# Kernel tuning notes

Hardware: AMD Instinct MI355X
Metric: run time of the kernel (lower is better)

The kernel has to match this reference:

```python
import jax, jax.numpy as jnp
import numpy as np

WS = 7      # window_size
NH = 8      # num_heads
ND = 5      # n_degree -> Np = 6


def setup_inputs() -> dict:
    key = jax.random.key(0)
    ks = jax.random.split(key, 9)
    B, Q, C, H, W = 2, 100, 256, 64, 64
    Np = ND + 1
    ws2 = WS * WS
    return {
        "x": jax.random.normal(ks[0], (B, C, H, W), dtype=jnp.float32),
        "polys": jax.random.uniform(ks[1], (B, Q, 2, Np), dtype=jnp.float32),
        "w_qkv": jax.random.normal(ks[2], (3 * C, C), dtype=jnp.float32) * 0.02,
        "b_qkv": jnp.zeros((3 * C,), dtype=jnp.float32),
        "w_proj": jax.random.normal(ks[3], (C, C), dtype=jnp.float32) * 0.02,
        "b_proj": jnp.zeros((C,), dtype=jnp.float32),
        "conv_w": jax.random.normal(ks[4], (1, ws2, 1, 1), dtype=jnp.float32) * 0.1,
        "conv_b": jnp.zeros((1,), dtype=jnp.float32),
        "pos_bias": jax.random.normal(ks[5], (ws2, 1), dtype=jnp.float32),
    }


def reference(x, polys, w_qkv, b_qkv, w_proj, b_proj, conv_w, conv_b, pos_bias):
    B, C, H, W = x.shape
    _, Q, _, Np = polys.shape  # polys: [B,Q,2,n_degree+1]
    ws = WS
    ws2 = ws * ws
    nh = NH
    hd = C // nh
    scale = hd ** -0.5

    # --- polynomial -> sample points (get_points) ---
    alpha = jnp.linspace(0.0, 1.0, Np)
    alphas = jnp.stack([alpha ** i for i in range(Np - 1, -1, -1)], axis=1)  # [Np, Np]
    points = jnp.swapaxes(polys @ alphas.T, -1, -2)  # [B,Q,Np,2]
    points = 2.0 * points - 1.0
    points = points[:, :, None, :, :]  # [B,Q,1,Np,2]

    # --- deformable window grid (faithful to torch, incl. -ws//2 floor-div) ---
    lo = (-ws) // 2   # -4 for ws=7
    hi = ws // 2      #  3
    delta_h = 2.0 * jnp.linspace(lo, hi, ws) / H
    delta_w = 2.0 * jnp.linspace(lo, hi, ws) / W
    mesh_x, mesh_y = jnp.meshgrid(delta_w, delta_h, indexing='xy')  # [ws,ws]
    mesh_x = mesh_x.reshape(-1, 1)  # [ws2,1]
    mesh_y = mesh_y.reshape(-1, 1)
    grid_y = points[..., 0] + mesh_y  # [B,Q,ws2,Np]
    grid_x = points[..., 1] + mesh_x
    grid = jnp.stack((grid_y, grid_x), axis=-1)        # [B,Q,ws2,Np,2]
    grid = grid.reshape(B, Q * Np * ws2, 2)            # same flat order as torch .view

    # --- grid_sample: bilinear, zeros padding, align_corners=True ---
    # grid[...,0] -> x coordinate (width), grid[...,1] -> y (height)
    def sample_one(img, g):  # img [C,H,W], g [P,2] -> [C,P]
        fx = (g[:, 0] + 1.0) * 0.5 * (W - 1)
        fy = (g[:, 1] + 1.0) * 0.5 * (H - 1)
        x0 = jnp.floor(fx)
        y0 = jnp.floor(fy)
        wx1 = fx - x0
        wy1 = fy - y0

        def gather(yy, xx):
            valid = (xx >= 0) & (xx <= W - 1) & (yy >= 0) & (yy <= H - 1)
            xi = jnp.clip(xx, 0, W - 1).astype(jnp.int32)
            yi = jnp.clip(yy, 0, H - 1).astype(jnp.int32)
            return img[:, yi, xi] * valid.astype(img.dtype)  # [C,P]

        v00 = gather(y0, x0)
        v01 = gather(y0, x0 + 1)
        v10 = gather(y0 + 1, x0)
        v11 = gather(y0 + 1, x0 + 1)
        return (v00 * (1 - wy1) * (1 - wx1) + v01 * (1 - wy1) * wx1 +
                v10 * wy1 * (1 - wx1) + v11 * wy1 * wx1)

    sampled = jax.vmap(sample_one)(x, grid)            # [B, C, Q*Np*ws2]
    sampled = sampled.reshape(B, C, Q * Np, ws2)
    sampled = jnp.transpose(sampled, (0, 2, 1, 3))     # [B, Q*Np, C, ws2]
    sp = sampled.reshape(B, Q, Np, C, ws2)
    sp = jnp.transpose(sp, (0, 1, 2, 4, 3)).reshape(B, Q * Np, ws2, C)

    # --- windowed multi-head self-attention over each sampled patch ---
    qkv = sp @ w_qkv.T + b_qkv                          # [B,QN,ws2,3C]
    qkv = qkv.reshape(B, Q * Np, ws2, 3, nh, hd)
    qkv = jnp.transpose(qkv, (3, 0, 4, 1, 2, 5))        # [3,B,nh,QN,ws2,hd]
    q, k, v = qkv[0], qkv[1], qkv[2]
    attn = jnp.einsum('bhnpd,bhnqd->bhnpq', q, k) * scale
    attn = attn + pos_bias.reshape(1, 1, 1, ws2, 1)     # bias per query row (as in torch)
    attn = jax.nn.softmax(attn, axis=-1)
    o = jnp.einsum('bhnpq,bhnqd->bhnpd', attn, v)       # [B,nh,QN,ws2,hd]
    o = jnp.swapaxes(o, 2, 3)                           # [B,nh,ws2,QN,hd]
    o = o.reshape(B, Q * Np, ws2, C)                    # faithful torch .reshape
    o = jnp.swapaxes(o, 1, 2)                           # [B,ws2,QN,C]

    # --- conv1x1 over the ws2 channel axis, then output projection ---
    y = jnp.einsum('bwnc,w->bnc', o, conv_w.reshape(ws2)) + conv_b.reshape(1, 1, 1)
    y = y @ w_proj.T + b_proj                           # [B,QN,C]
    return y.reshape(B, Q, Np, C)
```

## Files before the change

kernel.cpp:

```cpp
#include <hip/hip_runtime.h>
#include <hip/hip_bf16.h>

#define B_    2
#define QN    100
#define NP    6
#define WS2   49
#define CC    256
#define NHH   8
#define HDD   32
#define NWIN  600
#define O_PER_B 7526400

#define XT_BYTES   (8388608 + 1024)
#define ZABS       2097152
#define WB_BYTES   393216
#define WPT_BYTES  262144
#define QKV_SHORTS_PER_WIN (WS2 * 768)
#define QKV_BYTES  (1200 * WS2 * 768 * 2)

#define SPB_LD 264
#define CW_LD  72

typedef __attribute__((ext_vector_type(8))) short bf16x8;
typedef __attribute__((ext_vector_type(4))) float f32x4;

__device__ __forceinline__ unsigned short f2bf(float f) {
  union { float f; unsigned int i; } v; v.f = f;
  unsigned int x = v.i;
  x += 0x7fffu + ((x >> 16) & 1u);
  return (unsigned short)(x >> 16);
}
__device__ __forceinline__ float bf2f(unsigned short u) {
  union { unsigned int i; float f; } v; v.i = ((unsigned int)u) << 16; return v.f;
}

__global__ void k0_prep(const float* __restrict__ x, float* __restrict__ xT,
                        const float* __restrict__ w_qkv, unsigned short* __restrict__ wbp,
                        const float* __restrict__ w_proj, float* __restrict__ wpT) {
  __shared__ float tile[32][33];
  const int gb = blockIdx.x;
  if (gb < 2048) {
    int b   = gb >> 10;
    int rem = gb & 1023;
    int hw0 = (rem & 127) * 32;
    int c0  = (rem >> 7) * 32;
    int tx = threadIdx.x & 31, ty = threadIdx.x >> 5;
    const float* src = x + (size_t)b * CC * 4096;
    float* dst = xT + (size_t)b * 4096 * CC;
    #pragma unroll
    for (int i = ty; i < 32; i += 8)
      tile[i][tx] = src[(size_t)(c0 + i) * 4096 + hw0 + tx];
    __syncthreads();
    #pragma unroll
    for (int i = ty; i < 32; i += 8)
      dst[(size_t)(hw0 + i) * CC + c0 + tx] = tile[tx][i];
  } else if (gb < 2144) {
    int g = (gb - 2048) * 256 + threadIdx.x;
    int lane = g & 63;
    int ks = (g >> 6) & 7;
    int nt = g >> 9;
    int n  = nt * 16 + (lane & 15);
    int k0 = ks * 32 + (lane >> 4) * 8;
    const float* src = w_qkv + (size_t)n * CC + k0;
    float4 lo = *(const float4*)(src);
    float4 hi = *(const float4*)(src + 4);
    unsigned short o[8] = { f2bf(lo.x), f2bf(lo.y), f2bf(lo.z), f2bf(lo.w),
                            f2bf(hi.x), f2bf(hi.y), f2bf(hi.z), f2bf(hi.w) };
    *(uint4*)(wbp + (size_t)g * 8) = *(uint4*)o;
  } else if (gb == 2144) {
    xT[ZABS + threadIdx.x] = 0.0f;
  } else {
    int t = gb - 2145;
    int r0 = (t >> 3) * 32;
    int c0 = (t & 7) * 32;
    int tx = threadIdx.x & 31, ty = threadIdx.x >> 5;
    #pragma unroll
    for (int i = ty; i < 32; i += 8)
      tile[i][tx] = w_proj[(size_t)(r0 + i) * CC + c0 + tx];
    __syncthreads();
    #pragma unroll
    for (int i = ty; i < 32; i += 8)
      wpT[(size_t)(c0 + i) * CC + r0 + tx] = tile[tx][i];
  }
}

__launch_bounds__(256, 3)
__global__ void k1_sample_qkv(const float* __restrict__ xT,
                              const float* __restrict__ polys,
                              const unsigned short* __restrict__ wbp,
                              const float* __restrict__ b_qkv,
                              unsigned short* __restrict__ qkv_ws) {
  __shared__ __align__(16) unsigned short spb[64 * SPB_LD];
  __shared__ __align__(16) unsigned short Cwbuf[4][16 * CW_LD];
  __shared__ __align__(16) int   co_off[WS2][4];
  __shared__ __align__(16) float co_w[WS2][4];
  const int tid = threadIdx.x;
  const int m = blockIdx.x;
  const int b = blockIdx.y;

  if (tid < WS2) {
    int n = m * WS2 + tid;
    int q = n / (WS2 * NP);
    int p = (n / NP) % WS2;
    int a = n % NP;
    const float* pc = polys + (size_t)(b * QN + q) * 12;
    float al = (float)a * 0.2f;
    float py = pc[0];
    float px = pc[6];
    #pragma unroll
    for (int i = 1; i < 6; i++) { py = py * al + pc[i]; px = px * al + pc[6 + i]; }
    py = 2.0f * py - 1.0f;
    px = 2.0f * px - 1.0f;
    float gy = py + (2.0f * (-4.0f + (float)(p / 7) * (7.0f / 6.0f))) * (1.0f / 64.0f);
    float gx = px + (2.0f * (-4.0f + (float)(p % 7) * (7.0f / 6.0f))) * (1.0f / 64.0f);
    float fx = (gy + 1.0f) * 0.5f * 63.0f;
    float fy = (gx + 1.0f) * 0.5f * 63.0f;
    float x0 = floorf(fx), y0 = floorf(fy);
    float wx = fx - x0, wy = fy - y0;
    float x1 = x0 + 1.0f, y1 = y0 + 1.0f;
    int xi0 = (int)fminf(fmaxf(x0, 0.0f), 63.0f);
    int yi0 = (int)fminf(fmaxf(y0, 0.0f), 63.0f);
    int xi1 = (int)fminf(fmaxf(x1, 0.0f), 63.0f);
    int yi1 = (int)fminf(fmaxf(y1, 0.0f), 63.0f);
    bool vx0 = (x0 >= 0.0f) && (x0 <= 63.0f);
    bool vx1 = (x1 >= 0.0f) && (x1 <= 63.0f);
    bool vy0 = (y0 >= 0.0f) && (y0 <= 63.0f);
    bool vy1 = (y1 >= 0.0f) && (y1 <= 63.0f);
    const int bb = b * 4096;
    co_off[tid][0] = (vx0 && vy0) ? (bb + yi0 * 64 + xi0) * CC : ZABS;
    co_off[tid][1] = (vx1 && vy0) ? (bb + yi0 * 64 + xi1) * CC : ZABS;
    co_off[tid][2] = (vx0 && vy1) ? (bb + yi1 * 64 + xi0) * CC : ZABS;
    co_off[tid][3] = (vx1 && vy1) ? (bb + yi1 * 64 + xi1) * CC : ZABS;
    co_w[tid][0] = (1.0f - wy) * (1.0f - wx);
    co_w[tid][1] = (1.0f - wy) * wx;
    co_w[tid][2] = wy * (1.0f - wx);
    co_w[tid][3] = wy * wx;
  }
  {
    unsigned int* z = (unsigned int*)(spb + WS2 * SPB_LD);
    for (int i = tid; i < 15 * SPB_LD / 2; i += 256) z[i] = 0u;
  }
  __syncthreads();

  for (int bi = 0; bi < 12; bi++) {
    const int rbase = bi * 4;
    float vv[4][4];
    #pragma unroll
    for (int k = 0; k < 4; k++) {
      int r = rbase + k;
      int4 off = *(const int4*)&co_off[r][0];
      vv[k][0] = xT[off.x + tid];
      vv[k][1] = xT[off.y + tid];
      vv[k][2] = xT[off.z + tid];
      vv[k][3] = xT[off.w + tid];
    }
    #pragma unroll
    for (int k = 0; k < 4; k++) {
      int r = rbase + k;
      float4 w = *(const float4*)&co_w[r][0];
      float s = vv[k][0] * w.x + vv[k][1] * w.y + vv[k][2] * w.z + vv[k][3] * w.w;
      spb[r * SPB_LD + tid] = f2bf(s);
    }
  }
  {
    int4 off = *(const int4*)&co_off[48][0];
    float4 w = *(const float4*)&co_w[48][0];
    float s = xT[off.x + tid] * w.x + xT[off.y + tid] * w.y
            + xT[off.z + tid] * w.z + xT[off.w + tid] * w.w;
    spb[48 * SPB_LD + tid] = f2bf(s);
  }
  __syncthreads();

  const int lane = tid & 63;
  const int wv = tid >> 6;
  const int lm = lane & 15;
  const int lg = lane >> 4;
  unsigned short* qd = qkv_ws + (size_t)(b * NWIN + m) * QKV_SHORTS_PER_WIN;
  unsigned short* Cw = &Cwbuf[wv][0];

  for (int jc = 0; jc < 3; jc++) {
    const int nt0 = wv * 12 + jc * 4;
    const int ncol0 = nt0 * 16 + lm;
    f32x4 acc[4][4];
    #pragma unroll
    for (int j4 = 0; j4 < 4; j4++) {
      float bias = b_qkv[ncol0 + j4 * 16];
      #pragma unroll
      for (int mt = 0; mt < 4; mt++) acc[mt][j4] = (f32x4){bias, bias, bias, bias};
    }
    bf16x8 bnx[4];
    #pragma unroll
    for (int j4 = 0; j4 < 4; j4++)
      bnx[j4] = *(const bf16x8*)(wbp + (size_t)(((nt0 + j4) * 8 + 0) * 64 + lane) * 8);
    #pragma unroll
    for (int ks = 0; ks < 8; ks++) {
      bf16x8 bc[4];
      #pragma unroll
      for (int j4 = 0; j4 < 4; j4++) bc[j4] = bnx[j4];
      if (ks < 7) {
        #pragma unroll
        for (int j4 = 0; j4 < 4; j4++)
          bnx[j4] = *(const bf16x8*)(wbp + (size_t)(((nt0 + j4) * 8 + ks + 1) * 64 + lane) * 8);
      }
      bf16x8 af[4];
      #pragma unroll
      for (int mt = 0; mt < 4; mt++)
        af[mt] = *(const bf16x8*)(spb + (mt * 16 + lm) * SPB_LD + ks * 32 + lg * 8);
      #pragma unroll
      for (int j4 = 0; j4 < 4; j4++)
        #pragma unroll
        for (int mt = 0; mt < 4; mt++)
          acc[mt][j4] = __builtin_amdgcn_mfma_f32_16x16x32_bf16(af[mt], bc[j4], acc[mt][j4], 0, 0, 0);
    }
    const int cbase = nt0 * 16;
    #pragma unroll
    for (int mt = 0; mt < 4; mt++) {
      #pragma unroll
      for (int reg = 0; reg < 4; reg++) {
        int rr = lg * 4 + reg;
        #pragma unroll
        for (int j4 = 0; j4 < 4; j4++)
          Cw[rr * CW_LD + j4 * 16 + lm] = f2bf(acc[mt][j4][reg]);
      }
      int r0 = mt * 16;
      #pragma unroll
      for (int half = 0; half < 2; half++) {
        int idx = half * 64 + lane;
        int r16 = idx >> 3;
        int seg = idx & 7;
        int r = r0 + r16;
        if (r < WS2)
          *(uint4*)(qd + (size_t)r * 768 + cbase + seg * 8) =
              *(const uint4*)(Cw + r16 * CW_LD + seg * 8);
      }
    }
  }
}

#define P_LD 72
#define V_LD 72
#define OW_LD 36
#define P_WAVE (WS2 * P_LD)
#define V_OFF  (4 * P_WAVE)
#define V_WAVE (32 * V_LD)

__device__ __forceinline__ void attn_head(
    const bf16x8 qf[4], const bf16x8 kf[4],
    unsigned short* P, unsigned short* Vt, float* Ow, unsigned short* ob16,
    int lane, int lm, int lg) {
  const float scale = 0.17677669529663687f;
  f32x4 s[4][4];
  #pragma unroll
  for (int mt = 0; mt < 4; mt++)
    #pragma unroll
    for (int nt = 0; nt < 4; nt++) {
      s[mt][nt] = (f32x4){0.f, 0.f, 0.f, 0.f};
      s[mt][nt] = __builtin_amdgcn_mfma_f32_16x16x32_bf16(qf[mt], kf[nt], s[mt][nt], 0, 0, 0);
    }
  #pragma unroll
  for (int mt = 0; mt < 4; mt++)
    #pragma unroll
    for (int nt = 0; nt < 4; nt++) {
      bool badcol = (nt == 3) && (lm > 0);
      #pragma unroll
      for (int reg = 0; reg < 4; reg++)
        s[mt][nt][reg] = badcol ? -1e30f : s[mt][nt][reg] * scale;
    }
  #pragma unroll
  for (int mt = 0; mt < 4; mt++) {
    #pragma unroll
    for (int reg = 0; reg < 4; reg++) {
      float mx = fmaxf(fmaxf(s[mt][0][reg], s[mt][1][reg]),
                       fmaxf(s[mt][2][reg], s[mt][3][reg]));
      #pragma unroll
      for (int off = 1; off < 16; off <<= 1) mx = fmaxf(mx, __shfl_xor(mx, off));
      float sum = 0.0f;
      #pragma unroll
      for (int nt = 0; nt < 4; nt++) {
        float e = __expf(s[mt][nt][reg] - mx);
        s[mt][nt][reg] = e;
        sum += e;
      }
      #pragma unroll
      for (int off = 1; off < 16; off <<= 1) sum += __shfl_xor(sum, off);
      float inv = 1.0f / sum;
      #pragma unroll
      for (int nt = 0; nt < 4; nt++) s[mt][nt][reg] *= inv;
    }
  }
  #pragma unroll
  for (int mt = 0; mt < 4; mt++)
    #pragma unroll
    for (int nt = 0; nt < 4; nt++)
      #pragma unroll
      for (int reg = 0; reg < 4; reg++) {
        int p = mt * 16 + lg * 4 + reg;
        if (p < WS2) P[p * P_LD + nt * 16 + lm] = f2bf(s[mt][nt][reg]);
      }
  f32x4 o[4][2];
  #pragma unroll
  for (int mt = 0; mt < 4; mt++)
    #pragma unroll
    for (int nt2 = 0; nt2 < 2; nt2++) o[mt][nt2] = (f32x4){0.f, 0.f, 0.f, 0.f};
  #pragma unroll
  for (int ks = 0; ks < 2; ks++) {
    bf16x8 vf[2];
    #pragma unroll
    for (int nt2 = 0; nt2 < 2; nt2++)
      vf[nt2] = *(const bf16x8*)(Vt + (nt2 * 16 + lm) * V_LD + ks * 32 + lg * 8);
    #pragma unroll
    for (int mt = 0; mt < 4; mt++) {
      bf16x8 af = *(const bf16x8*)(P + (mt * 16 + lm) * P_LD + ks * 32 + lg * 8);
      #pragma unroll
      for (int nt2 = 0; nt2 < 2; nt2++)
        o[mt][nt2] = __builtin_amdgcn_mfma_f32_16x16x32_bf16(af, vf[nt2], o[mt][nt2], 0, 0, 0);
    }
  }
  #pragma unroll
  for (int mt = 0; mt < 4; mt++)
    #pragma unroll
    for (int reg = 0; reg < 4; reg++) {
      int p = mt * 16 + lg * 4 + reg;
      if (p < WS2) {
        #pragma unroll
        for (int nt2 = 0; nt2 < 2; nt2++)
          Ow[p * OW_LD + nt2 * 16 + lm] = o[mt][nt2][reg];
      }
    }
  for (int idx = lane; idx < WS2 * 4; idx += 64) {
    int p = idx >> 2, seg = idx & 3;
    const float* src = Ow + p * OW_LD + seg * 8;
    unsigned short o8[8];
    #pragma unroll
    for (int k = 0; k < 8; k++) o8[k] = f2bf(src[k]);
    *(uint4*)(ob16 + (size_t)idx * 8) = *(uint4*)o8;
  }
}

__launch_bounds__(256, 3)
__global__ void k2_attn(const unsigned short* __restrict__ qkv_ws,
                        unsigned short* __restrict__ o16) {
  __shared__ __align__(16) unsigned short lds[V_OFF + 4 * V_WAVE];
  const int tid = threadIdx.x;
  const int lane = tid & 63;
  const int wv = tid >> 6;
  const int lm = lane & 15;
  const int lg = lane >> 4;
  const int m = blockIdx.x;
  const int b = blockIdx.y;
  const unsigned short* wsrc = qkv_ws + (size_t)(b * NWIN + m) * QKV_SHORTS_PER_WIN;
  unsigned short* P  = lds + wv * P_WAVE;
  unsigned short* Vt = lds + V_OFF + wv * V_WAVE;
  float* Ow = (float*)P;

  {
    unsigned int* vz = (unsigned int*)Vt;
    #pragma unroll
    for (int i = 0; i < 18; i++) vz[i * 64 + lane] = 0u;
  }

  const int h0 = 2 * wv, h1 = 2 * wv + 1;
  const int vr = lane >> 2;
  const int vd0 = (lane & 3) * 8;
  uint4 vbuf[4];
  #pragma unroll
  for (int i = 0; i < 4; i++) {
    int r = vr + i * 16;
    int rc = (r > 48) ? 48 : r;
    vbuf[i] = *(const uint4*)(wsrc + (size_t)rc * 768 + 512 + h0 * HDD + vd0);
  }
  bf16x8 qf[2][4], kf[2][4];
  #pragma unroll
  for (int t = 0; t < 4; t++) {
    int r = t * 16 + lm; if (r > 48) r = 48;
    qf[0][t] = *(const bf16x8*)(wsrc + (size_t)r * 768 + h0 * HDD + lg * 8);
    kf[0][t] = *(const bf16x8*)(wsrc + (size_t)r * 768 + 256 + h0 * HDD + lg * 8);
    qf[1][t] = *(const bf16x8*)(wsrc + (size_t)r * 768 + h1 * HDD + lg * 8);
    kf[1][t] = *(const bf16x8*)(wsrc + (size_t)r * 768 + 256 + h1 * HDD + lg * 8);
  }
  #pragma unroll
  for (int i = 0; i < 4; i++) {
    int r = vr + i * 16;
    if (r < WS2) {
      unsigned int uu[4] = { vbuf[i].x, vbuf[i].y, vbuf[i].z, vbuf[i].w };
      #pragma unroll
      for (int k = 0; k < 4; k++) {
        Vt[(vd0 + 2 * k) * V_LD + r]     = (unsigned short)(uu[k] & 0xffffu);
        Vt[(vd0 + 2 * k + 1) * V_LD + r] = (unsigned short)(uu[k] >> 16);
      }
    }
  }

  unsigned short* obase = o16 + ((size_t)(b * NWIN + m) * 392) * 32;
  unsigned short* ob0 = obase + (size_t)h0 * WS2 * HDD;
  unsigned short* ob1 = obase + (size_t)h1 * WS2 * HDD;

  uint4 vbuf2[4];
  #pragma unroll
  for (int i = 0; i < 4; i++) {
    int r = vr + i * 16;
    int rc = (r > 48) ? 48 : r;
    vbuf2[i] = *(const uint4*)(wsrc + (size_t)rc * 768 + 512 + h1 * HDD + vd0);
  }

  attn_head(qf[0], kf[0], P, Vt, Ow, ob0, lane, lm, lg);

  #pragma unroll
  for (int i = 0; i < 4; i++) {
    int r = vr + i * 16;
    if (r < WS2) {
      unsigned int uu[4] = { vbuf2[i].x, vbuf2[i].y, vbuf2[i].z, vbuf2[i].w };
      #pragma unroll
      for (int k = 0; k < 4; k++) {
        Vt[(vd0 + 2 * k) * V_LD + r]     = (unsigned short)(uu[k] & 0xffffu);
        Vt[(vd0 + 2 * k + 1) * V_LD + r] = (unsigned short)(uu[k] >> 16);
      }
    }
  }

  attn_head(qf[1], kf[1], P, Vt, Ow, ob1, lane, lm, lg);
}

__global__ void k3_conv_proj(const unsigned short* __restrict__ o16,
                             const float* __restrict__ conv_w,
                             const float* __restrict__ conv_b,
                             const float* __restrict__ wpT,
                             const float* __restrict__ b_proj,
                             float* __restrict__ out) {
  __shared__ float yv[CC];
  __shared__ float cw[WS2];
  __shared__ int atab[392];
  const int tid = threadIdx.x;
  const int np = blockIdx.x;
  const int b = blockIdx.y;
  if (tid < WS2) cw[tid] = conv_w[tid];
  for (int i = tid; i < 392; i += 256) {
    int Q = np * 392 + i;
    int m = Q % 600;
    int hp = Q / 600;
    atab[i] = ((b * NWIN + m) * 392 + hp) * 32;
  }
  __syncthreads();
  const int cg = tid >> 5, dd = tid & 31;
  float acc = conv_b[0];
  for (int p = 0; p < WS2; p++)
    acc += cw[p] * bf2f(o16[(size_t)atab[p * 8 + cg] + dd]);
  yv[tid] = acc;
  __syncthreads();
  const float* wp = wpT + tid;
  float a0 = 0.0f, a1 = 0.0f, a2 = 0.0f, a3 = 0.0f;
  #pragma unroll 8
  for (int c = 0; c < CC; c += 4) {
    float4 y4 = *(const float4*)&yv[c];
    a0 += y4.x * wp[(c + 0) * CC];
    a1 += y4.y * wp[(c + 1) * CC];
    a2 += y4.z * wp[(c + 2) * CC];
    a3 += y4.w * wp[(c + 3) * CC];
  }
  out[((size_t)(b * NWIN + np)) * CC + tid] = b_proj[tid] + ((a0 + a1) + (a2 + a3));
}

extern "C" void kernel_launch(void* const* d_in, const int* in_sizes, int n_in,
                              void* d_out, int out_size, void* d_ws, size_t ws_size,
                              hipStream_t stream) {
  const float* x        = (const float*)d_in[0];
  const float* polys    = (const float*)d_in[1];
  const float* w_qkv    = (const float*)d_in[2];
  const float* b_qkv    = (const float*)d_in[3];
  const float* w_proj   = (const float*)d_in[4];
  const float* b_proj   = (const float*)d_in[5];
  const float* conv_w   = (const float*)d_in[6];
  const float* conv_b   = (const float*)d_in[7];
  float* out = (float*)d_out;

  char* ws = (char*)d_ws;
  float* xT = (float*)ws;
  unsigned short* wbp = (unsigned short*)(ws + XT_BYTES);
  float* wpT = (float*)(ws + XT_BYTES + WB_BYTES);
  unsigned short* qkv_ws = (unsigned short*)(ws + XT_BYTES + WB_BYTES + WPT_BYTES);
  unsigned short* o16 = (unsigned short*)(ws + XT_BYTES + WB_BYTES + WPT_BYTES + QKV_BYTES);

  hipLaunchKernelGGL(k0_prep, dim3(2209), dim3(256), 0, stream, x, xT, w_qkv, wbp, w_proj, wpT);
  hipLaunchKernelGGL(k1_sample_qkv, dim3(NWIN, B_), dim3(256), 0, stream,
                     xT, polys, wbp, b_qkv, qkv_ws);
  hipLaunchKernelGGL(k2_attn, dim3(NWIN, B_), dim3(256), 0, stream,
                     qkv_ws, o16);
  hipLaunchKernelGGL(k3_conv_proj, dim3(NWIN, B_), dim3(256), 0, stream,
                     o16, conv_w, conv_b, wpT, b_proj, out);
}
```

Before: 170.9 us.

## Fuse sampling/QKV projection with windowed attention, keeping QKV in LDS

Merges the sample+QKV kernel and the attention kernel into one, so each wave computes the Q/K/V columns for its own two heads and keeps them in shared memory, with V stored transposed directly from the accumulators. This removes the global round-trip of the bf16 QKV buffer (about 58 MB written and read back) and one kernel launch. The sampling loop also batches 8 rows of gathers instead of 4 to raise memory-level parallelism. In exchange LDS use per block grows and launch bounds drop to one block per SIMD group hint, which may lower occupancy.

```diff
diff --git a/kernel.cpp b/kernel.cpp
--- a/kernel.cpp
+++ b/kernel.cpp
@@ -1,5 +1,4 @@
 #include <hip/hip_runtime.h>
-#include <hip/hip_bf16.h>
 
 #define B_    2
 #define QN    100
@@ -9,17 +8,20 @@
 #define NHH   8
 #define HDD   32
 #define NWIN  600
-#define O_PER_B 7526400
 
 #define XT_BYTES   (8388608 + 1024)
 #define ZABS       2097152
 #define WB_BYTES   393216
 #define WPT_BYTES  262144
-#define QKV_SHORTS_PER_WIN (WS2 * 768)
-#define QKV_BYTES  (1200 * WS2 * 768 * 2)
 
 #define SPB_LD 264
-#define CW_LD  72
+
+#define QW_LD  136
+#define VT_LD  72
+#define P_LD   72
+#define OW_LD  36
+#define QW_SHORTS   (WS2 * QW_LD)
+#define WREG_SHORTS (QW_SHORTS + 64 * VT_LD)
 
 typedef __attribute__((ext_vector_type(8))) short bf16x8;
 typedef __attribute__((ext_vector_type(4))) float f32x4;
@@ -84,19 +86,118 @@
   }
 }
 
-__launch_bounds__(256, 3)
-__global__ void k1_sample_qkv(const float* __restrict__ xT,
-                              const float* __restrict__ polys,
-                              const unsigned short* __restrict__ wbp,
-                              const float* __restrict__ b_qkv,
-                              unsigned short* __restrict__ qkv_ws) {
+__device__ __forceinline__ void attn_head(
+    const bf16x8 qf[4], const bf16x8 kf[4],
+    unsigned short* P, const unsigned short* Vt, float* Ow, unsigned short* ob16,
+    int lane, int lm, int lg) {
+  const float scale = 0.17677669529663687f;
+  f32x4 s[4][4];
+  #pragma unroll
+  for (int mt = 0; mt < 4; mt++)
+    #pragma unroll
+    for (int nt = 0; nt < 4; nt++) {
+      s[mt][nt] = (f32x4){0.f, 0.f, 0.f, 0.f};
+      s[mt][nt] = __builtin_amdgcn_mfma_f32_16x16x32_bf16(qf[mt], kf[nt], s[mt][nt], 0, 0, 0);
+    }
+  #pragma unroll
+  for (int mt = 0; mt < 4; mt++)
+    #pragma unroll
+    for (int nt = 0; nt < 4; nt++) {
+      bool badcol = (nt == 3) && (lm > 0);
+      #pragma unroll
+      for (int reg = 0; reg < 4; reg++)
+        s[mt][nt][reg] = badcol ? -1e30f : s[mt][nt][reg] * scale;
+    }
+  #pragma unroll
+  for (int mt = 0; mt < 4; mt++) {
+    #pragma unroll
+    for (int reg = 0; reg < 4; reg++) {
+      float mx = fmaxf(fmaxf(s[mt][0][reg], s[mt][1][reg]),
+                       fmaxf(s[mt][2][reg], s[mt][3][reg]));
+      #pragma unroll
+      for (int off = 1; off < 16; off <<= 1) mx = fmaxf(mx, __shfl_xor(mx, off));
+      float sum = 0.0f;
+      #pragma unroll
+      for (int nt = 0; nt < 4; nt++) {
+        float e = __expf(s[mt][nt][reg] - mx);
+        s[mt][nt][reg] = e;
+        sum += e;
+      }
+      #pragma unroll
+      for (int off = 1; off < 16; off <<= 1) sum += __shfl_xor(sum, off);
+      float inv = 1.0f / sum;
+      #pragma unroll
+      for (int nt = 0; nt < 4; nt++) s[mt][nt][reg] *= inv;
+    }
+  }
+  #pragma unroll
+  for (int mt = 0; mt < 4; mt++)
+    #pragma unroll
+    for (int nt = 0; nt < 4; nt++)
+      #pragma unroll
+      for (int reg = 0; reg < 4; reg++) {
+        int p = mt * 16 + lg * 4 + reg;
+        if (p < WS2) P[p * P_LD + nt * 16 + lm] = f2bf(s[mt][nt][reg]);
+      }
+  f32x4 o[4][2];
+  #pragma unroll
+  for (int mt = 0; mt < 4; mt++)
+    #pragma unroll
+    for (int nt2 = 0; nt2 < 2; nt2++) o[mt][nt2] = (f32x4){0.f, 0.f, 0.f, 0.f};
+  #pragma unroll
+  for (int ks = 0; ks < 2; ks++) {
+    bf16x8 vf[2];
+    #pragma unroll
+    for (int nt2 = 0; nt2 < 2; nt2++)
+      vf[nt2] = *(const bf16x8*)(Vt + (nt2 * 16 + lm) * VT_LD + ks * 32 + lg * 8);
+    #pragma unroll
+    for (int mt = 0; mt < 4; mt++) {
+      bf16x8 af = *(const bf16x8*)(P + (mt * 16 + lm) * P_LD + ks * 32 + lg * 8);
+      #pragma unroll
+      for (int nt2 = 0; nt2 < 2; nt2++)
+        o[mt][nt2] = __builtin_amdgcn_mfma_f32_16x16x32_bf16(af, vf[nt2], o[mt][nt2], 0, 0, 0);
+    }
+  }
+  #pragma unroll
+  for (int mt = 0; mt < 4; mt++)
+    #pragma unroll
+    for (int reg = 0; reg < 4; reg++) {
+      int p = mt * 16 + lg * 4 + reg;
+      if (p < WS2) {
+        #pragma unroll
+        for (int nt2 = 0; nt2 < 2; nt2++)
+          Ow[p * OW_LD + nt2 * 16 + lm] = o[mt][nt2][reg];
+      }
+    }
+  for (int idx = lane; idx < WS2 * 4; idx += 64) {
+    int p = idx >> 2, seg = idx & 3;
+    const float* src = Ow + p * OW_LD + seg * 8;
+    unsigned short o8[8];
+    #pragma unroll
+    for (int k = 0; k < 8; k++) o8[k] = f2bf(src[k]);
+    *(uint4*)(ob16 + (size_t)idx * 8) = *(uint4*)o8;
+  }
+}
+
+__launch_bounds__(256, 1)
+__global__ void k12_fused(const float* __restrict__ xT,
+                          const float* __restrict__ polys,
+                          const unsigned short* __restrict__ wbp,
+                          const float* __restrict__ b_qkv,
+                          unsigned short* __restrict__ o16) {
   __shared__ __align__(16) unsigned short spb[64 * SPB_LD];
-  __shared__ __align__(16) unsigned short Cwbuf[4][16 * CW_LD];
+  __shared__ __align__(16) unsigned short wreg[4][WREG_SHORTS];
   __shared__ __align__(16) int   co_off[WS2][4];
   __shared__ __align__(16) float co_w[WS2][4];
   const int tid = threadIdx.x;
   const int m = blockIdx.x;
   const int b = blockIdx.y;
+  const int lane = tid & 63;
+  const int wv = tid >> 6;
+  const int lm = lane & 15;
+  const int lg = lane >> 4;
+  unsigned short* myq = &wreg[wv][0];
+  unsigned short* VtW = myq + QW_SHORTS;
 
   if (tid < WS2) {
     int n = m * WS2 + tid;
@@ -140,13 +241,18 @@
     unsigned int* z = (unsigned int*)(spb + WS2 * SPB_LD);
     for (int i = tid; i < 15 * SPB_LD / 2; i += 256) z[i] = 0u;
   }
+  {
+    unsigned int* vz = (unsigned int*)VtW;
+    #pragma unroll
+    for (int i = 0; i < 36; i++) vz[i * 64 + lane] = 0u;
+  }
   __syncthreads();
 
-  for (int bi = 0; bi < 12; bi++) {
-    const int rbase = bi * 4;
-    float vv[4][4];
-    #pragma unroll
-    for (int k = 0; k < 4; k++) {
+  for (int bi = 0; bi < 6; bi++) {
+    const int rbase = bi * 8;
+    float vv[8][4];
+    #pragma unroll
+    for (int k = 0; k < 8; k++) {
       int r = rbase + k;
       int4 off = *(const int4*)&co_off[r][0];
       vv[k][0] = xT[off.x + tid];
@@ -155,7 +261,7 @@
       vv[k][3] = xT[off.w + tid];
     }
     #pragma unroll
-    for (int k = 0; k < 4; k++) {
+    for (int k = 0; k < 8; k++) {
       int r = rbase + k;
       float4 w = *(const float4*)&co_w[r][0];
       float s = vv[k][0] * w.x + vv[k][1] * w.y + vv[k][2] * w.z + vv[k][3] * w.w;
@@ -171,15 +277,8 @@
   }
   __syncthreads();
 
-  const int lane = tid & 63;
-  const int wv = tid >> 6;
-  const int lm = lane & 15;
-  const int lg = lane >> 4;
-  unsigned short* qd = qkv_ws + (size_t)(b * NWIN + m) * QKV_SHORTS_PER_WIN;
-  unsigned short* Cw = &Cwbuf[wv][0];
-
   for (int jc = 0; jc < 3; jc++) {
-    const int nt0 = wv * 12 + jc * 4;
+    const int nt0 = jc * 16 + wv * 4;
     const int ncol0 = nt0 * 16 + lm;
     f32x4 acc[4][4];
     #pragma unroll
@@ -212,213 +311,51 @@
         for (int mt = 0; mt < 4; mt++)
           acc[mt][j4] = __builtin_amdgcn_mfma_f32_16x16x32_bf16(af[mt], bc[j4], acc[mt][j4], 0, 0, 0);
     }
-    const int cbase = nt0 * 16;
-    #pragma unroll
-    for (int mt = 0; mt < 4; mt++) {
-      #pragma unroll
-      for (int reg = 0; reg < 4; reg++) {
-        int rr = lg * 4 + reg;
+    if (jc < 2) {
+      const int cb = jc * 64;
+      #pragma unroll
+      for (int mt = 0; mt < 4; mt++)
         #pragma unroll
-        for (int j4 = 0; j4 < 4; j4++)
-          Cw[rr * CW_LD + j4 * 16 + lm] = f2bf(acc[mt][j4][reg]);
-      }
-      int r0 = mt * 16;
-      #pragma unroll
-      for (int half = 0; half < 2; half++) {
-        int idx = half * 64 + lane;
-        int r16 = idx >> 3;
-        int seg = idx & 7;
-        int r = r0 + r16;
-        if (r < WS2)
-          *(uint4*)(qd + (size_t)r * 768 + cbase + seg * 8) =
-              *(const uint4*)(Cw + r16 * CW_LD + seg * 8);
-      }
-    }
-  }
-}
-
-#define P_LD 72
-#define V_LD 72
-#define OW_LD 36
-#define P_WAVE (WS2 * P_LD)
-#define V_OFF  (4 * P_WAVE)
-#define V_WAVE (32 * V_LD)
-
-__device__ __forceinline__ void attn_head(
-    const bf16x8 qf[4], const bf16x8 kf[4],
-    unsigned short* P, unsigned short* Vt, float* Ow, unsigned short* ob16,
-    int lane, int lm, int lg) {
-  const float scale = 0.17677669529663687f;
-  f32x4 s[4][4];
-  #pragma unroll
-  for (int mt = 0; mt < 4; mt++)
-    #pragma unroll
-    for (int nt = 0; nt < 4; nt++) {
-      s[mt][nt] = (f32x4){0.f, 0.f, 0.f, 0.f};
-      s[mt][nt] = __builtin_amdgcn_mfma_f32_16x16x32_bf16(qf[mt], kf[nt], s[mt][nt], 0, 0, 0);
-    }
-  #pragma unroll
-  for (int mt = 0; mt < 4; mt++)
-    #pragma unroll
-    for (int nt = 0; nt < 4; nt++) {
-      bool badcol = (nt == 3) && (lm > 0);
-      #pragma unroll
-      for (int reg = 0; reg < 4; reg++)
-        s[mt][nt][reg] = badcol ? -1e30f : s[mt][nt][reg] * scale;
-    }
-  #pragma unroll
-  for (int mt = 0; mt < 4; mt++) {
-    #pragma unroll
-    for (int reg = 0; reg < 4; reg++) {
-      float mx = fmaxf(fmaxf(s[mt][0][reg], s[mt][1][reg]),
-                       fmaxf(s[mt][2][reg], s[mt][3][reg]));
-      #pragma unroll
-      for (int off = 1; off < 16; off <<= 1) mx = fmaxf(mx, __shfl_xor(mx, off));
-      float sum = 0.0f;
-      #pragma unroll
-      for (int nt = 0; nt < 4; nt++) {
-        float e = __expf(s[mt][nt][reg] - mx);
-        s[mt][nt][reg] = e;
-        sum += e;
-      }
-      #pragma unroll
-      for (int off = 1; off < 16; off <<= 1) sum += __shfl_xor(sum, off);
-      float inv = 1.0f / sum;
-      #pragma unroll
-      for (int nt = 0; nt < 4; nt++) s[mt][nt][reg] *= inv;
-    }
-  }
-  #pragma unroll
-  for (int mt = 0; mt < 4; mt++)
-    #pragma unroll
-    for (int nt = 0; nt < 4; nt++)
-      #pragma unroll
-      for (int reg = 0; reg < 4; reg++) {
-        int p = mt * 16 + lg * 4 + reg;
-        if (p < WS2) P[p * P_LD + nt * 16 + lm] = f2bf(s[mt][nt][reg]);
-      }
-  f32x4 o[4][2];
-  #pragma unroll
-  for (int mt = 0; mt < 4; mt++)
-    #pragma unroll
-    for (int nt2 = 0; nt2 < 2; nt2++) o[mt][nt2] = (f32x4){0.f, 0.f, 0.f, 0.f};
-  #pragma unroll
-  for (int ks = 0; ks < 2; ks++) {
-    bf16x8 vf[2];
-    #pragma unroll
-    for (int nt2 = 0; nt2 < 2; nt2++)
-      vf[nt2] = *(const bf16x8*)(Vt + (nt2 * 16 + lm) * V_LD + ks * 32 + lg * 8);
-    #pragma unroll
-    for (int mt = 0; mt < 4; mt++) {
-      bf16x8 af = *(const bf16x8*)(P + (mt * 16 + lm) * P_LD + ks * 32 + lg * 8);
-      #pragma unroll
-      for (int nt2 = 0; nt2 < 2; nt2++)
-        o[mt][nt2] = __builtin_amdgcn_mfma_f32_16x16x32_bf16(af, vf[nt2], o[mt][nt2], 0, 0, 0);
-    }
-  }
-  #pragma unroll
-  for (int mt = 0; mt < 4; mt++)
-    #pragma unroll
-    for (int reg = 0; reg < 4; reg++) {
-      int p = mt * 16 + lg * 4 + reg;
-      if (p < WS2) {
+        for (int reg = 0; reg < 4; reg++) {
+          int rr = mt * 16 + lg * 4 + reg;
+          if (rr < WS2) {
+            #pragma unroll
+            for (int j4 = 0; j4 < 4; j4++)
+              myq[rr * QW_LD + cb + j4 * 16 + lm] = f2bf(acc[mt][j4][reg]);
+          }
+        }
+    } else {
+      #pragma unroll
+      for (int mt = 0; mt < 4; mt++)
         #pragma unroll
-        for (int nt2 = 0; nt2 < 2; nt2++)
-          Ow[p * OW_LD + nt2 * 16 + lm] = o[mt][nt2][reg];
-      }
-    }
-  for (int idx = lane; idx < WS2 * 4; idx += 64) {
-    int p = idx >> 2, seg = idx & 3;
-    const float* src = Ow + p * OW_LD + seg * 8;
-    unsigned short o8[8];
-    #pragma unroll
-    for (int k = 0; k < 8; k++) o8[k] = f2bf(src[k]);
-    *(uint4*)(ob16 + (size_t)idx * 8) = *(uint4*)o8;
-  }
-}
-
-__launch_bounds__(256, 3)
-__global__ void k2_attn(const unsigned short* __restrict__ qkv_ws,
-                        unsigned short* __restrict__ o16) {
-  __shared__ __align__(16) unsigned short lds[V_OFF + 4 * V_WAVE];
-  const int tid = threadIdx.x;
-  const int lane = tid & 63;
-  const int wv = tid >> 6;
-  const int lm = lane & 15;
-  const int lg = lane >> 4;
-  const int m = blockIdx.x;
-  const int b = blockIdx.y;
-  const unsigned short* wsrc = qkv_ws + (size_t)(b * NWIN + m) * QKV_SHORTS_PER_WIN;
-  unsigned short* P  = lds + wv * P_WAVE;
-  unsigned short* Vt = lds + V_OFF + wv * V_WAVE;
-  float* Ow = (float*)P;
-
-  {
-    unsigned int* vz = (unsigned int*)Vt;
-    #pragma unroll
-    for (int i = 0; i < 18; i++) vz[i * 64 + lane] = 0u;
-  }
-
-  const int h0 = 2 * wv, h1 = 2 * wv + 1;
-  const int vr = lane >> 2;
-  const int vd0 = (lane & 3) * 8;
-  uint4 vbuf[4];
-  #pragma unroll
-  for (int i = 0; i < 4; i++) {
-    int r = vr + i * 16;
-    int rc = (r > 48) ? 48 : r;
-    vbuf[i] = *(const uint4*)(wsrc + (size_t)rc * 768 + 512 + h0 * HDD + vd0);
-  }
+        for (int reg = 0; reg < 4; reg++) {
+          int rr = mt * 16 + lg * 4 + reg;
+          if (rr < WS2) {
+            #pragma unroll
+            for (int j4 = 0; j4 < 4; j4++)
+              VtW[(j4 * 16 + lm) * VT_LD + rr] = f2bf(acc[mt][j4][reg]);
+          }
+        }
+    }
+  }
+
   bf16x8 qf[2][4], kf[2][4];
   #pragma unroll
   for (int t = 0; t < 4; t++) {
     int r = t * 16 + lm; if (r > 48) r = 48;
-    qf[0][t] = *(const bf16x8*)(wsrc + (size_t)r * 768 + h0 * HDD + lg * 8);
-    kf[0][t] = *(const bf16x8*)(wsrc + (size_t)r * 768 + 256 + h0 * HDD + lg * 8);
-    qf[1][t] = *(const bf16x8*)(wsrc + (size_t)r * 768 + h1 * HDD + lg * 8);
-    kf[1][t] = *(const bf16x8*)(wsrc + (size_t)r * 768 + 256 + h1 * HDD + lg * 8);
-  }
-  #pragma unroll
-  for (int i = 0; i < 4; i++) {
-    int r = vr + i * 16;
-    if (r < WS2) {
-      unsigned int uu[4] = { vbuf[i].x, vbuf[i].y, vbuf[i].z, vbuf[i].w };
-      #pragma unroll
-      for (int k = 0; k < 4; k++) {
-        Vt[(vd0 + 2 * k) * V_LD + r]     = (unsigned short)(uu[k] & 0xffffu);
-        Vt[(vd0 + 2 * k + 1) * V_LD + r] = (unsigned short)(uu[k] >> 16);
-      }
-    }
-  }
-
-  unsigned short* obase = o16 + ((size_t)(b * NWIN + m) * 392) * 32;
-  unsigned short* ob0 = obase + (size_t)h0 * WS2 * HDD;
-  unsigned short* ob1 = obase + (size_t)h1 * WS2 * HDD;
-
-  uint4 vbuf2[4];
-  #pragma unroll
-  for (int i = 0; i < 4; i++) {
-    int r = vr + i * 16;
-    int rc = (r > 48) ? 48 : r;
-    vbuf2[i] = *(const uint4*)(wsrc + (size_t)rc * 768 + 512 + h1 * HDD + vd0);
-  }
-
-  attn_head(qf[0], kf[0], P, Vt, Ow, ob0, lane, lm, lg);
-
-  #pragma unroll
-  for (int i = 0; i < 4; i++) {
-    int r = vr + i * 16;
-    if (r < WS2) {
-      unsigned int uu[4] = { vbuf2[i].x, vbuf2[i].y, vbuf2[i].z, vbuf2[i].w };
-      #pragma unroll
-      for (int k = 0; k < 4; k++) {
-        Vt[(vd0 + 2 * k) * V_LD + r]     = (unsigned short)(uu[k] & 0xffffu);
-        Vt[(vd0 + 2 * k + 1) * V_LD + r] = (unsigned short)(uu[k] >> 16);
-      }
-    }
-  }
-
-  attn_head(qf[1], kf[1], P, Vt, Ow, ob1, lane, lm, lg);
+    const unsigned short* row = myq + r * QW_LD;
+    qf[0][t] = *(const bf16x8*)(row + lg * 8);
+    kf[0][t] = *(const bf16x8*)(row + 64 + lg * 8);
+    qf[1][t] = *(const bf16x8*)(row + 32 + lg * 8);
+    kf[1][t] = *(const bf16x8*)(row + 96 + lg * 8);
+  }
+  unsigned short* P = myq;
+  float* Ow = (float*)myq;
+  unsigned short* obase = o16 + (size_t)(b * NWIN + m) * 392 * 32;
+  attn_head(qf[0], kf[0], P, VtW, Ow,
+            obase + (size_t)(2 * wv) * WS2 * HDD, lane, lm, lg);
+  attn_head(qf[1], kf[1], P, VtW + 32 * VT_LD, Ow,
+            obase + (size_t)(2 * wv + 1) * WS2 * HDD, lane, lm, lg);
 }
 
 __global__ void k3_conv_proj(const unsigned short* __restrict__ o16,
@@ -477,14 +414,11 @@
   float* xT = (float*)ws;
   unsigned short* wbp = (unsigned short*)(ws + XT_BYTES);
   float* wpT = (float*)(ws + XT_BYTES + WB_BYTES);
-  unsigned short* qkv_ws = (unsigned short*)(ws + XT_BYTES + WB_BYTES + WPT_BYTES);
-  unsigned short* o16 = (unsigned short*)(ws + XT_BYTES + WB_BYTES + WPT_BYTES + QKV_BYTES);
+  unsigned short* o16 = (unsigned short*)(ws + XT_BYTES + WB_BYTES + WPT_BYTES);
 
   hipLaunchKernelGGL(k0_prep, dim3(2209), dim3(256), 0, stream, x, xT, w_qkv, wbp, w_proj, wpT);
-  hipLaunchKernelGGL(k1_sample_qkv, dim3(NWIN, B_), dim3(256), 0, stream,
-                     xT, polys, wbp, b_qkv, qkv_ws);
-  hipLaunchKernelGGL(k2_attn, dim3(NWIN, B_), dim3(256), 0, stream,
-                     qkv_ws, o16);
+  hipLaunchKernelGGL(k12_fused, dim3(NWIN, B_), dim3(256), 0, stream,
+                     xT, polys, wbp, b_qkv, o16);
   hipLaunchKernelGGL(k3_conv_proj, dim3(NWIN, B_), dim3(256), 0, stream,
                      o16, conv_w, conv_b, wpT, b_proj, out);
 }
```

Result: slower. 233.8 us (+36.8%).
